# Kernel tuning notes

Measured on AMD Instinct MI355X. Metric: run time of the kernel, lower is better.

Reference implementation:

```python
import jax, jax.numpy as jnp
import numpy as np

B, T, C, K = 1024, 500, 64, 2000  # batch, timesteps, latent chains (KCs), observed KCs
S, O = 2, 2                       # n_states, n_outputs (hard-coded in BktModel)


def setup_inputs() -> dict:
    key = jax.random.key(0)
    k1, k2, k3, k4, k5, k6 = jax.random.split(key, 6)
    corr = jax.random.randint(k1, (B, T), 0, O)
    kc = jax.random.randint(k2, (B, T), 0, K)
    # soft KC-membership matrix (stands in for gumbel_softmax sample; rows sum to 1)
    A = jax.nn.softmax(jax.random.normal(k3, (K, C)), axis=1)
    trans_logits = jax.random.normal(k4, (C, S, S))
    obs_logits = jax.random.normal(k5, (C, S, O))
    init_logits = jax.random.normal(k6, (C, S))
    return dict(corr=corr, kc=kc, A=A, trans_logits=trans_logits,
                obs_logits=obs_logits, init_logits=init_logits)


def _hmm_forward(obs, chain, trans_logits, obs_logits, init_logits):
    # obs: [B,T] int, chain: [B,T,C] float
    n_batch = obs.shape[0]
    log_obs = jax.nn.log_softmax(obs_logits, axis=2)   # [C,S,O]
    log_t = jax.nn.log_softmax(trans_logits, axis=1)   # [C,S,S] (normalized over dim 1, as in torch)
    log_alpha0 = jnp.tile(jax.nn.log_softmax(init_logits, axis=1)[None], (n_batch, 1, 1))  # [B,C,S]

    def step(log_alpha, xs):
        y, cc = xs  # y: [B] int, cc: [B,C]
        # predictive distribution over outputs
        a1 = jnp.einsum('bc,cso->bso', cc, log_obs)          # [B,S,O]
        a2 = jnp.einsum('bc,bcs->bs', cc, log_alpha)         # [B,S]
        log_py = jax.scipy.special.logsumexp(a1 + a2[:, :, None], axis=1)  # [B,O]
        log_py = jax.nn.log_softmax(log_py, axis=1)
        # state update for the active chains
        lo_y = jnp.transpose(log_obs[:, :, y], (2, 0, 1))    # [B,C,S]
        lp = jnp.einsum('bcs,bc->bs', lo_y, cc)              # [B,S]
        a1c = jnp.einsum('bcs,bc->bs', log_alpha, cc)        # [B,S]
        a2c = jnp.einsum('bc,cst->bst', cc, log_t)           # [B,S,S]
        a3 = jax.scipy.special.logsumexp(lp[:, None, :] + a1c[:, None, :] + a2c, axis=2)  # [B,S]
        new_la = (1.0 - cc)[:, :, None] * log_alpha + cc[:, :, None] * a3[:, None, :]
        return new_la, log_py

    _, outs = jax.lax.scan(step, log_alpha0,
                           (obs.T, jnp.transpose(chain, (1, 0, 2))))
    return jnp.transpose(outs, (1, 0, 2))  # [B,T,O]


def reference(corr, kc, A, trans_logits, obs_logits, init_logits):
    chain = A[kc]  # [B,T,C]
    return _hmm_forward(corr, chain, trans_logits, obs_logits, init_logits)
```

## Files before the change

kernel.cpp:

```cpp
#include <hip/hip_runtime.h>
#include <math.h>

#define BB 1024
#define TT 500
#define CC_ 64
#define KK 2000

#define LOG2E 1.44269504088896340736f
#define LN2   0.69314718055994530942f

#if __has_builtin(__builtin_amdgcn_exp2f)
__device__ __forceinline__ float fast_exp2(float x) { return __builtin_amdgcn_exp2f(x); }
#else
__device__ __forceinline__ float fast_exp2(float x) { return exp2f(x); }
#endif
#if __has_builtin(__builtin_amdgcn_logf)
__device__ __forceinline__ float fast_log2(float x) { return __builtin_amdgcn_logf(x); }
#else
__device__ __forceinline__ float fast_log2(float x) { return log2f(x); }
#endif

__device__ __forceinline__ float lse2_2(float a, float b) {
    float m = fmaxf(a, b);
    float d = fminf(a, b) - m;
    return m + fast_log2(1.0f + fast_exp2(d));
}

template<int CTRL, int RM, int BM>
__device__ __forceinline__ float dpp_add(float x) {
    int s = __builtin_amdgcn_update_dpp(0, __float_as_int(x), CTRL, RM, BM, true);
    return x + __int_as_float(s);
}
__device__ __forceinline__ float wave_sum63(float x) {
    x = dpp_add<0x111, 0xf, 0xf>(x);
    x = dpp_add<0x112, 0xf, 0xf>(x);
    x = dpp_add<0x114, 0xf, 0xf>(x);
    x = dpp_add<0x118, 0xf, 0xf>(x);
    x = dpp_add<0x142, 0xa, 0xf>(x);
    x = dpp_add<0x143, 0xc, 0xf>(x);
    return x;
}
__device__ __forceinline__ float rowsum16(float x) {
    x = dpp_add<0x121, 0xf, 0xf>(x);
    x = dpp_add<0x122, 0xf, 0xf>(x);
    x = dpp_add<0x124, 0xf, 0xf>(x);
    x = dpp_add<0x128, 0xf, 0xf>(x);
    return x;
}

__global__ __launch_bounds__(64) void precompute_P(
    const float* __restrict__ A,
    const float* __restrict__ trans_logits,
    const float* __restrict__ obs_logits,
    float* __restrict__ PA,
    float* __restrict__ P3)
{
    int k = blockIdx.x;
    int c = threadIdx.x;

    float ob[2][2];
#pragma unroll
    for (int s = 0; s < 2; ++s) {
        float o0 = obs_logits[c * 4 + s * 2 + 0] * LOG2E;
        float o1 = obs_logits[c * 4 + s * 2 + 1] * LOG2E;
        float l = lse2_2(o0, o1);
        ob[s][0] = o0 - l;
        ob[s][1] = o1 - l;
    }
    float lt[2][2];
    {
        float t00 = trans_logits[c * 4 + 0] * LOG2E;
        float t01 = trans_logits[c * 4 + 1] * LOG2E;
        float t10 = trans_logits[c * 4 + 2] * LOG2E;
        float t11 = trans_logits[c * 4 + 3] * LOG2E;
        float l0 = lse2_2(t00, t10);
        float l1 = lse2_2(t01, t11);
        lt[0][0] = t00 - l0; lt[0][1] = t01 - l1;
        lt[1][0] = t10 - l0; lt[1][1] = t11 - l1;
    }

    float a = A[k * CC_ + c];
    float v[8];
    v[0] = a * ob[0][0]; v[1] = a * ob[0][1];
    v[2] = a * ob[1][0]; v[3] = a * ob[1][1];
    v[4] = a * lt[0][0]; v[5] = a * lt[0][1];
    v[6] = a * lt[1][0]; v[7] = a * lt[1][1];

#pragma unroll
    for (int i = 0; i < 8; ++i) v[i] = wave_sum63(v[i]);
    if (c == 63) {
        ((float4*)PA)[k] = make_float4(v[0], v[1], v[2], v[3]);
#pragma unroll
        for (int y = 0; y < 2; ++y) {
            float sel0 = v[y];
            float sel1 = v[2 + y];
            ((float4*)P3)[k * 2 + y] = make_float4(
                fast_exp2(sel0 + v[4]),
                fast_exp2(sel0 + v[6]),
                sel1 + v[5],
                sel1 + v[7]);
        }
    }
}

__global__ __launch_bounds__(64) void bkt_main(
    const int* __restrict__ corr,
    const int* __restrict__ kc,
    const float* __restrict__ A,
    const float* __restrict__ init_logits,
    const float* __restrict__ P3,
    float* __restrict__ out)
{
    int lane = threadIdx.x;
    int g = lane >> 4, i = lane & 15;
    int b = blockIdx.x * 4 + g;

    float la[4][2];
#pragma unroll
    for (int j = 0; j < 4; ++j) {
        float i0 = init_logits[(4 * i + j) * 2 + 0] * LOG2E;
        float i1 = init_logits[(4 * i + j) * 2 + 1] * LOG2E;
        float l = lse2_2(i0, i1);
        la[j][0] = i0 - l;
        la[j][1] = i1 - l;
    }

    const int* kcb = kc + b * TT;
    const int* cb  = corr + b * TT;
    float2* outb   = (float2*)(out + (size_t)b * TT * 2);

    int kq[16], yq[16];
#pragma unroll
    for (int q = 0; q < 16; ++q) { kq[q] = kcb[q]; yq[q] = cb[q]; }

    float4 ccq[8], pq[8];
#pragma unroll
    for (int q = 0; q < 6; ++q) {
        ccq[q] = *(const float4*)(A + kq[q] * CC_ + 4 * i);
        pq[q]  = ((const float4*)P3)[kq[q] * 2 + yq[q]];
    }

    for (int tt = 0; tt <= 496; tt += 16) {
#pragma unroll
        for (int j = 0; j < 16; ++j) {
            int t = tt + j;
            int t16 = t + 16; if (t16 > TT - 1) t16 = TT - 1;
            int knew = kcb[t16];
            int ynew = cb[t16];
            int kp = kq[(j + 6) & 15], yp = yq[(j + 6) & 15];
            ccq[(j + 6) & 7] = *(const float4*)(A + kp * CC_ + 4 * i);
            pq[(j + 6) & 7]  = ((const float4*)P3)[kp * 2 + yp];

            float4 cc = ccq[j & 7];
            float4 pr = pq[j & 7];
            kq[j] = knew; yq[j] = ynew;

            float x0 = (cc.x * la[0][0] + cc.y * la[1][0])
                     + (cc.z * la[2][0] + cc.w * la[3][0]);
            float x1 = (cc.x * la[0][1] + cc.y * la[1][1])
                     + (cc.z * la[2][1] + cc.w * la[3][1]);
            x0 = rowsum16(x0);
            x1 = rowsum16(x1);
            if (t < TT && i == 0) outb[t] = make_float2(x0, x1);

            float d   = x1 - x0;
            float a30 = fast_log2(pr.x + fast_exp2(pr.z + d));
            float a31 = fast_log2(pr.y + fast_exp2(pr.w + d));
            {
                float g0, g1;
                g0 = la[0][0] - x0; g1 = la[0][1] - x0;
                la[0][0] = g0 + cc.x * (a30 - g0);
                la[0][1] = g1 + cc.x * (a31 - g1);
                g0 = la[1][0] - x0; g1 = la[1][1] - x0;
                la[1][0] = g0 + cc.y * (a30 - g0);
                la[1][1] = g1 + cc.y * (a31 - g1);
                g0 = la[2][0] - x0; g1 = la[2][1] - x0;
                la[2][0] = g0 + cc.z * (a30 - g0);
                la[2][1] = g1 + cc.z * (a31 - g1);
                g0 = la[3][0] - x0; g1 = la[3][1] - x0;
                la[3][0] = g0 + cc.w * (a30 - g0);
                la[3][1] = g1 + cc.w * (a31 - g1);
            }
        }
    }
}

__global__ __launch_bounds__(256) void finish_py(
    const int* __restrict__ kc,
    const float* __restrict__ PA,
    float* __restrict__ out)
{
    int idx = blockIdx.x * 256 + threadIdx.x;
    if (idx >= BB * TT) return;
    int k = kc[idx];
    float2 r  = ((const float2*)out)[idx];
    float4 pa = ((const float4*)PA)[k];
    float lo0 = lse2_2(pa.x + r.x, pa.z + r.y);
    float lo1 = lse2_2(pa.y + r.x, pa.w + r.y);
    float lz  = lse2_2(lo0, lo1);
    ((float2*)out)[idx] = make_float2((lo0 - lz) * LN2, (lo1 - lz) * LN2);
}

extern "C" void kernel_launch(void* const* d_in, const int* in_sizes, int n_in,
                              void* d_out, int out_size, void* d_ws, size_t ws_size,
                              hipStream_t stream) {
    const int* corr    = (const int*)d_in[0];
    const int* kc      = (const int*)d_in[1];
    const float* A     = (const float*)d_in[2];
    const float* trans = (const float*)d_in[3];
    const float* obs   = (const float*)d_in[4];
    const float* init  = (const float*)d_in[5];
    float* out = (float*)d_out;

    float* PA = (float*)d_ws;
    float* P3 = PA + KK * 4;

    precompute_P<<<KK, 64, 0, stream>>>(A, trans, obs, PA, P3);
    bkt_main<<<BB / 4, 64, 0, stream>>>(corr, kc, A, init, P3, out);
    finish_py<<<(BB * TT + 255) / 256, 256, 0, stream>>>(kc, PA, out);
}
```

Measured before the change: 95.86 us.

## Hand-schedule prefetch loads with inline asm and partial vmcnt waits

Replaces compiler-generated global loads in the recurrence loop with inline-asm loads plus an explicit s_waitcnt vmcnt(30). Only the data for the current step has to arrive, while later prefetches stay in flight. The aim is to stop the compiler inserting conservative full waits that stall the serial per-timestep chain. The output store moves to the end of the step, is issued by all lanes, and also uses asm. The risk is that the waitcnt accounting is fragile: stores also count toward vmcnt, so a wrong count could read data that has not arrived yet. Launch bounds now also request a minimum of one block per multiprocessor.

```diff
diff --git a/kernel.cpp b/kernel.cpp
--- a/kernel.cpp
+++ b/kernel.cpp
@@ -8,6 +8,9 @@
 
 #define LOG2E 1.44269504088896340736f
 #define LN2   0.69314718055994530942f
+
+typedef float f32x4 __attribute__((ext_vector_type(4)));
+typedef float f32x2 __attribute__((ext_vector_type(2)));
 
 #if __has_builtin(__builtin_amdgcn_exp2f)
 __device__ __forceinline__ float fast_exp2(float x) { return __builtin_amdgcn_exp2f(x); }
@@ -103,7 +106,7 @@
     }
 }
 
-__global__ __launch_bounds__(64) void bkt_main(
+__global__ __launch_bounds__(64, 1) void bkt_main(
     const int* __restrict__ corr,
     const int* __restrict__ kc,
     const float* __restrict__ A,
@@ -114,6 +117,7 @@
     int lane = threadIdx.x;
     int g = lane >> 4, i = lane & 15;
     int b = blockIdx.x * 4 + g;
+    int bTT = b * TT;
 
     float la[4][2];
 #pragma unroll
@@ -125,35 +129,56 @@
         la[j][1] = i1 - l;
     }
 
-    const int* kcb = kc + b * TT;
-    const int* cb  = corr + b * TT;
-    float2* outb   = (float2*)(out + (size_t)b * TT * 2);
-
-    int kq[16], yq[16];
-#pragma unroll
-    for (int q = 0; q < 16; ++q) { kq[q] = kcb[q]; yq[q] = cb[q]; }
-
-    float4 ccq[8], pq[8];
+    int   kq[16], yq[16];
+    f32x4 ccq[8], pq[8];
+
+#pragma unroll
+    for (int q = 0; q < 16; ++q) {
+        int voff = (bTT + q) * 4;
+        asm volatile("global_load_dword %0, %2, %3\n\t"
+                     "global_load_dword %1, %2, %4"
+                     : "=&v"(kq[q]), "=&v"(yq[q])
+                     : "v"(voff), "s"(kc), "s"(corr));
+    }
+#pragma unroll
+    for (int q = 0; q < 16; ++q)
+        asm volatile("s_waitcnt vmcnt(0)" : "+v"(kq[q]), "+v"(yq[q]));
 #pragma unroll
     for (int q = 0; q < 6; ++q) {
-        ccq[q] = *(const float4*)(A + kq[q] * CC_ + 4 * i);
-        pq[q]  = ((const float4*)P3)[kq[q] * 2 + yq[q]];
-    }
+        int va = kq[q] * 256 + i * 16;
+        int vp = (kq[q] * 2 + yq[q]) * 16;
+        asm volatile("global_load_dwordx4 %0, %1, %2"
+                     : "=&v"(ccq[q]) : "v"(va), "s"(A));
+        asm volatile("global_load_dwordx4 %0, %1, %2"
+                     : "=&v"(pq[q]) : "v"(vp), "s"(P3));
+    }
+#pragma unroll
+    for (int q = 0; q < 6; ++q)
+        asm volatile("s_waitcnt vmcnt(0)" : "+v"(ccq[q]), "+v"(pq[q]));
 
     for (int tt = 0; tt <= 496; tt += 16) {
 #pragma unroll
         for (int j = 0; j < 16; ++j) {
             int t = tt + j;
             int t16 = t + 16; if (t16 > TT - 1) t16 = TT - 1;
-            int knew = kcb[t16];
-            int ynew = cb[t16];
-            int kp = kq[(j + 6) & 15], yp = yq[(j + 6) & 15];
-            ccq[(j + 6) & 7] = *(const float4*)(A + kp * CC_ + 4 * i);
-            pq[(j + 6) & 7]  = ((const float4*)P3)[kp * 2 + yp];
-
-            float4 cc = ccq[j & 7];
-            float4 pr = pq[j & 7];
-            kq[j] = knew; yq[j] = ynew;
+            int voff = (bTT + t16) * 4;
+            asm volatile("global_load_dword %0, %2, %3\n\t"
+                         "global_load_dword %1, %2, %4"
+                         : "=&v"(kq[j]), "=&v"(yq[j])
+                         : "v"(voff), "s"(kc), "s"(corr));
+            int k6 = kq[(j + 6) & 15], y6 = yq[(j + 6) & 15];
+            int va = k6 * 256 + i * 16;
+            int vp = (k6 * 2 + y6) * 16;
+            asm volatile("global_load_dwordx4 %0, %1, %2"
+                         : "=&v"(ccq[(j + 6) & 7]) : "v"(va), "s"(A));
+            asm volatile("global_load_dwordx4 %0, %1, %2"
+                         : "=&v"(pq[(j + 6) & 7]) : "v"(vp), "s"(P3));
+            asm volatile("s_waitcnt vmcnt(30)"
+                         : "+v"(ccq[j & 7]), "+v"(pq[j & 7]),
+                           "+v"(kq[(j + 7) & 15]), "+v"(yq[(j + 7) & 15]));
+
+            f32x4 cc = ccq[j & 7];
+            f32x4 pr = pq[j & 7];
 
             float x0 = (cc.x * la[0][0] + cc.y * la[1][0])
                      + (cc.z * la[2][0] + cc.w * la[3][0]);
@@ -161,7 +186,6 @@
                      + (cc.z * la[2][1] + cc.w * la[3][1]);
             x0 = rowsum16(x0);
             x1 = rowsum16(x1);
-            if (t < TT && i == 0) outb[t] = make_float2(x0, x1);
 
             float d   = x1 - x0;
             float a30 = fast_log2(pr.x + fast_exp2(pr.z + d));
@@ -181,6 +205,13 @@
                 la[3][0] = g0 + cc.w * (a30 - g0);
                 la[3][1] = g1 + cc.w * (a31 - g1);
             }
+
+            if (t < TT) {
+                f32x2 o; o.x = x0; o.y = x1;
+                int vo = (bTT + t) * 8;
+                asm volatile("global_store_dwordx2 %1, %0, %2"
+                             :: "v"(o), "v"(vo), "s"(out));
+            }
         }
     }
 }
```

After: 82.20 us, median of 2. -14.2%, faster.
